# Kernel tuning notes

Measured on AMD Instinct MI355X. Metric: run time of the kernel, lower is better.

The kernel has to match this reference:

```python
import jax, jax.numpy as jnp
import numpy as np

DIM = 256          # args.dim
MAX_Z = 100        # args.max_z
N_ATOM_EMBED = DIM - 1  # Euclidean manifold: dim - 1
B, N = 256, 128    # graphs, nodes per graph
E = B * N * N      # fully connected edges per batch, flattened
NORM_CONSTANT = 1.0


def setup_inputs() -> dict:
    key = jax.random.key(0)
    ks = jax.random.split(key, 8)
    x = jax.random.normal(ks[0], (B, N, 3), dtype=jnp.float32)
    categories = jax.random.randint(ks[1], (B, N), 0, MAX_Z)
    charges = jax.random.normal(ks[2], (B, N, 1), dtype=jnp.float32)
    edges = jax.random.randint(ks[3], (2, E), 0, B * N)
    node_mask = jnp.ones((B, N, 1), dtype=jnp.float32)
    edge_mask = jnp.ones((E, 1), dtype=jnp.float32)
    # nn.Embedding(max_z, n_atom_embed, padding_idx=0): row 0 is zeros
    emb = jax.random.normal(ks[4], (MAX_Z, N_ATOM_EMBED), dtype=jnp.float32)
    emb_table = emb.at[0].set(0.0)
    # nn.Linear(dim, 2*dim)
    lim = 1.0 / np.sqrt(DIM)
    W = jax.random.uniform(ks[5], (DIM, 2 * DIM), minval=-lim, maxval=lim, dtype=jnp.float32)
    b_lin = jax.random.uniform(ks[6], (2 * DIM,), minval=-lim, maxval=lim, dtype=jnp.float32)
    return {"x": x, "categories": categories, "charges": charges, "edges": edges,
            "node_mask": node_mask, "edge_mask": edge_mask,
            "emb_table": emb_table, "W": W, "b_lin": b_lin}


def coord2diff(x, edges, norm_constant=NORM_CONSTANT):
    row, col = edges[0], edges[1]
    coord_diff = x[row] - x[col]                              # [E, 3] gather + diff
    radial = jnp.sum(coord_diff * coord_diff, axis=1, keepdims=True)  # [E, 1]
    norm = jnp.sqrt(radial + 1e-8)
    coord_diff = coord_diff / (norm + norm_constant)
    return radial, coord_diff


def reference(x, categories, charges, edges, node_mask, edge_mask, emb_table, W, b_lin):
    h = emb_table[categories]                      # [B, N, dim-1] embedding lookup
    h = jnp.concatenate([charges, h], axis=2)      # [B, N, dim]
    b, n_nodes, d = h.shape
    xf = x.reshape(b * n_nodes, 3)
    nm = node_mask.reshape(b * n_nodes, 1)
    h = h.reshape(b * n_nodes, d) * nm             # masked node features
    radial, coord_diff = coord2diff(xf, edges)     # edge-index gather + norm
    # encode() pass-through (abstract layers treated as identity), then head
    parameters = h @ W + b_lin                     # [B*N, 2*dim] mean/logvar
    return parameters, radial, coord_diff
```

## Files before the change

### kernel.cpp

```cpp
#include <hip/hip_runtime.h>

typedef unsigned short u16;
typedef unsigned int u32;
typedef __attribute__((ext_vector_type(8))) short bf16x8;
typedef __attribute__((ext_vector_type(4))) float f32x4;

#define DIM 256
#define NOUT 512
#define MROWS 32768
#define NNODE 32768
#define NEDGE (256*128*128)
#define PARAM_SZ (32768*512)
#define GEMM_BLOCKS 512
#define EDGE_BLOCKS 4096

__device__ __forceinline__ u16 f2bf(float f) {
    u32 x = __float_as_uint(f);
    u32 r = (x + 0x7FFFu + ((x >> 16) & 1u)) >> 16;
    return (u16)r;
}
__device__ __forceinline__ float bf2f(u16 u) {
    union { u32 i; float f; } v; v.i = ((u32)u) << 16; return v.f;
}

__global__ __launch_bounds__(256) void prep_kernel(const float* __restrict__ W,
                                                   const float* __restrict__ x,
                                                   const float* __restrict__ emb,
                                                   u16* __restrict__ Wt,
                                                   float4* __restrict__ xp,
                                                   u16* __restrict__ embp) {
    const int b = blockIdx.x;
    const int tid = threadIdx.x;
    if (b < 128) {
        __shared__ u16 tile[32][33];
        int k0 = (b >> 4) * 32;
        int n0 = (b & 15) * 32;
        int tx = tid & 31, ty0 = tid >> 5;
        #pragma unroll
        for (int j = 0; j < 4; ++j) {
            int ty = ty0 + j * 8;
            tile[ty][tx] = f2bf(W[(k0 + ty) * NOUT + n0 + tx]);
        }
        __syncthreads();
        #pragma unroll
        for (int j = 0; j < 4; ++j) {
            int ty = ty0 + j * 8;
            Wt[(n0 + ty) * DIM + k0 + tx] = tile[tx][ty];
        }
    } else if (b < 256) {
        int i = (b - 128) * 256 + tid;
        float4 v;
        v.x = x[i * 3 + 0]; v.y = x[i * 3 + 1]; v.z = x[i * 3 + 2]; v.w = 0.0f;
        xp[i] = v;
    } else {
        int i = (b - 256) * 256 + tid;
        int col = i & 255;
        int row = i >> 8;
        embp[i] = (col == 0) ? (u16)0 : f2bf(emb[row * 255 + col - 1]);
    }
}

__device__ __forceinline__ void gather8_sc0(const float4* p0, const float4* p1,
                                            const float4* p2, const float4* p3,
                                            const float4* p4, const float4* p5,
                                            const float4* p6, const float4* p7,
                                            f32x4& a0, f32x4& a1, f32x4& a2, f32x4& a3,
                                            f32x4& b0, f32x4& b1, f32x4& b2, f32x4& b3) {
    asm volatile(
        "global_load_dwordx4 %0, %8, off sc0\n\t"
        "global_load_dwordx4 %1, %9, off sc0\n\t"
        "global_load_dwordx4 %2, %10, off sc0\n\t"
        "global_load_dwordx4 %3, %11, off sc0\n\t"
        "global_load_dwordx4 %4, %12, off sc0\n\t"
        "global_load_dwordx4 %5, %13, off sc0\n\t"
        "global_load_dwordx4 %6, %14, off sc0\n\t"
        "global_load_dwordx4 %7, %15, off sc0\n\t"
        "s_waitcnt vmcnt(0)"
        : "=&v"(a0), "=&v"(a1), "=&v"(a2), "=&v"(a3),
          "=&v"(b0), "=&v"(b1), "=&v"(b2), "=&v"(b3)
        : "v"(p0), "v"(p1), "v"(p2), "v"(p3), "v"(p4), "v"(p5), "v"(p6), "v"(p7)
        : "memory");
}

__device__ __forceinline__ void edge_part(int eb, int tid,
                                          const int* __restrict__ edges,
                                          const float4* __restrict__ xp,
                                          float* __restrict__ radial_out,
                                          float* __restrict__ cd_out,
                                          float* buf ) {
    const int t4 = eb * 256 + tid;
    int4 r4 = ((const int4*)edges)[t4];
    int4 c4 = ((const int4*)(edges + NEDGE))[t4];

    f32x4 xr0, xr1, xr2, xr3, xc0, xc1, xc2, xc3;
    gather8_sc0(xp + r4.x, xp + r4.y, xp + r4.z, xp + r4.w,
                xp + c4.x, xp + c4.y, xp + c4.z, xp + c4.w,
                xr0, xr1, xr2, xr3, xc0, xc1, xc2, xc3);

    f32x4 rad;
    float cdv[12];
    #pragma unroll
    for (int e = 0; e < 4; ++e) {
        f32x4 a = (e == 0) ? xr0 : (e == 1) ? xr1 : (e == 2) ? xr2 : xr3;
        f32x4 b = (e == 0) ? xc0 : (e == 1) ? xc1 : (e == 2) ? xc2 : xc3;
        float dx = a.x - b.x, dy = a.y - b.y, dz = a.z - b.z;
        float r = dx * dx + dy * dy + dz * dz;
        float inv = 1.0f / (sqrtf(r + 1e-8f) + 1.0f);
        rad[e] = r;
        cdv[e * 3 + 0] = dx * inv;
        cdv[e * 3 + 1] = dy * inv;
        cdv[e * 3 + 2] = dz * inv;
    }
    __builtin_nontemporal_store(rad, ((f32x4*)radial_out) + t4);

    #pragma unroll
    for (int k = 0; k < 3; ++k)
        ((f32x4*)buf)[tid * 3 + k] = ((const f32x4*)cdv)[k];
    __syncthreads();
    f32x4* cdg = (f32x4*)(cd_out + (size_t)eb * 3072);
    #pragma unroll
    for (int k = 0; k < 3; ++k)
        __builtin_nontemporal_store(((const f32x4*)buf)[k * 256 + tid], cdg + k * 256 + tid);
}

__device__ __forceinline__ void gemm_part(int gb, int tid,
                                          const int* __restrict__ cats,
                                          const float* __restrict__ charges,
                                          const float* __restrict__ nmask,
                                          const u16* __restrict__ embp,
                                          const u16* __restrict__ Wt,
                                          const float* __restrict__ bias,
                                          float* __restrict__ out,
                                          u16 (*h_lds)[DIM + 8]) {
    const int m0 = gb * 64;

    {
        int r = tid >> 2;
        int q = tid & 3;
        int m = m0 + r;
        float mask = nmask[m];
        const uint4* src = (const uint4*)(embp + (size_t)cats[m] * 256 + q * 64);
        uint4 v[8];
        #pragma unroll
        for (int t = 0; t < 8; ++t) v[t] = src[t];
        if (mask != 1.0f) {
            #pragma unroll
            for (int t = 0; t < 8; ++t) {
                u32* w = (u32*)&v[t];
                #pragma unroll
                for (int j = 0; j < 4; ++j) {
                    u16 lo = f2bf(bf2f((u16)(w[j] & 0xFFFF)) * mask);
                    u16 hi = f2bf(bf2f((u16)(w[j] >> 16)) * mask);
                    w[j] = (u32)lo | ((u32)hi << 16);
                }
            }
        }
        if (q == 0) {
            u32* w0 = (u32*)&v[0];
            w0[0] = (w0[0] & 0xFFFF0000u) | (u32)f2bf(charges[m] * mask);
        }
        #pragma unroll
        for (int t = 0; t < 8; ++t)
            *(uint4*)&h_lds[r][q * 64 + t * 8] = v[t];
    }
    __syncthreads();

    const int wave = tid >> 6;
    const int lane = tid & 63;
    const int lrow = lane & 15;
    const int quad = lane >> 4;
    const int nbase = wave * 128;

    f32x4 acc[4][8];
    #pragma unroll
    for (int ms = 0; ms < 4; ++ms)
        #pragma unroll
        for (int nt = 0; nt < 8; ++nt) acc[ms][nt] = (f32x4)(0.0f);

    #pragma unroll
    for (int k0 = 0; k0 < DIM; k0 += 32) {
        bf16x8 a[4];
        #pragma unroll
        for (int ms = 0; ms < 4; ++ms)
            a[ms] = *(const bf16x8*)&h_lds[ms * 16 + lrow][k0 + quad * 8];
        #pragma unroll
        for (int nt = 0; nt < 8; ++nt) {
            bf16x8 bfr = *(const bf16x8*)&Wt[(size_t)(nbase + nt * 16 + lrow) * DIM + k0 + quad * 8];
            #pragma unroll
            for (int ms = 0; ms < 4; ++ms)
                acc[ms][nt] = __builtin_amdgcn_mfma_f32_16x16x32_bf16(a[ms], bfr, acc[ms][nt], 0, 0, 0);
        }
    }

    #pragma unroll
    for (int nt = 0; nt < 8; ++nt) {
        int n = nbase + nt * 16 + lrow;
        float bv = bias[n];
        #pragma unroll
        for (int ms = 0; ms < 4; ++ms)
            #pragma unroll
            for (int r = 0; r < 4; ++r)
                __builtin_nontemporal_store(acc[ms][nt][r] + bv,
                    out + (size_t)(m0 + ms * 16 + quad * 4 + r) * NOUT + n);
    }
}

__global__ __launch_bounds__(256, 2) void main_kernel(const int* __restrict__ cats,
                                                      const float* __restrict__ charges,
                                                      const float* __restrict__ nmask,
                                                      const u16* __restrict__ embp,
                                                      const u16* __restrict__ Wt,
                                                      const float* __restrict__ bias,
                                                      const int* __restrict__ edges,
                                                      const float4* __restrict__ xp,
                                                      float* __restrict__ params,
                                                      float* __restrict__ radial,
                                                      float* __restrict__ cd) {
    __shared__ char smem[64 * (DIM + 8) * sizeof(u16)];
    if (blockIdx.x < GEMM_BLOCKS)
        gemm_part(blockIdx.x, threadIdx.x, cats, charges, nmask, embp, Wt, bias, params,
                  (u16 (*)[DIM + 8])smem);
    else
        edge_part(blockIdx.x - GEMM_BLOCKS, threadIdx.x, edges, xp, radial, cd,
                  (float*)smem);
}

extern "C" void kernel_launch(void* const* d_in, const int* in_sizes, int n_in,
                              void* d_out, int out_size, void* d_ws, size_t ws_size,
                              hipStream_t stream) {
    const float* x       = (const float*)d_in[0];
    const int*   cats    = (const int*)d_in[1];
    const float* charges = (const float*)d_in[2];
    const int*   edges   = (const int*)d_in[3];
    const float* nmask   = (const float*)d_in[4];
    const float* emb     = (const float*)d_in[6];
    const float* W       = (const float*)d_in[7];
    const float* bias    = (const float*)d_in[8];

    float* out    = (float*)d_out;
    float* params = out;
    float* radial = out + PARAM_SZ;
    float* cd     = out + PARAM_SZ + NEDGE;

    u16*    Wt   = (u16*)d_ws;
    float4* xp   = (float4*)((char*)d_ws + 256 * 1024);
    u16*    embp = (u16*)((char*)d_ws + 768 * 1024);

    prep_kernel<<<356, 256, 0, stream>>>(W, x, emb, Wt, xp, embp);
    main_kernel<<<GEMM_BLOCKS + EDGE_BLOCKS, 256, 0, stream>>>(
        cats, charges, nmask, embp, Wt, bias, edges, xp, params, radial, cd);
}
```

Measured before the change: 232.7 us.

## Split fused GEMM/edge kernel into separate edge and GEMM launches

Replaces the single heterogeneous kernel, which branched on block index between GEMM and edge work, with two separate kernels launched back to back on the same stream. Each kernel now gets its own register allocation, LDS size and launch bounds, so the lightweight edge kernel is no longer limited by the GEMM's resource footprint and can reach higher occupancy. The cost is an extra launch and losing the overlap between GEMM and edge work within one grid.

```diff
diff --git a/kernel.cpp b/kernel.cpp
--- a/kernel.cpp
+++ b/kernel.cpp
@@ -82,12 +82,13 @@
         : "memory");
 }
 
-__device__ __forceinline__ void edge_part(int eb, int tid,
-                                          const int* __restrict__ edges,
-                                          const float4* __restrict__ xp,
-                                          float* __restrict__ radial_out,
-                                          float* __restrict__ cd_out,
-                                          float* buf ) {
+__global__ __launch_bounds__(256) void edge_kernel(const int* __restrict__ edges,
+                                                   const float4* __restrict__ xp,
+                                                   float* __restrict__ radial_out,
+                                                   float* __restrict__ cd_out) {
+    __shared__ float buf[3072];
+    const int eb = blockIdx.x;
+    const int tid = threadIdx.x;
     const int t4 = eb * 256 + tid;
     int4 r4 = ((const int4*)edges)[t4];
     int4 c4 = ((const int4*)(edges + NEDGE))[t4];
@@ -123,15 +124,16 @@
         __builtin_nontemporal_store(((const f32x4*)buf)[k * 256 + tid], cdg + k * 256 + tid);
 }
 
-__device__ __forceinline__ void gemm_part(int gb, int tid,
-                                          const int* __restrict__ cats,
-                                          const float* __restrict__ charges,
-                                          const float* __restrict__ nmask,
-                                          const u16* __restrict__ embp,
-                                          const u16* __restrict__ Wt,
-                                          const float* __restrict__ bias,
-                                          float* __restrict__ out,
-                                          u16 (*h_lds)[DIM + 8]) {
+__global__ __launch_bounds__(256, 2) void gemm_kernel(const int* __restrict__ cats,
+                                                      const float* __restrict__ charges,
+                                                      const float* __restrict__ nmask,
+                                                      const u16* __restrict__ embp,
+                                                      const u16* __restrict__ Wt,
+                                                      const float* __restrict__ bias,
+                                                      float* __restrict__ out) {
+    __shared__ u16 h_lds[64][DIM + 8];
+    const int gb = blockIdx.x;
+    const int tid = threadIdx.x;
     const int m0 = gb * 64;
 
     {
@@ -205,26 +207,6 @@
     }
 }
 
-__global__ __launch_bounds__(256, 2) void main_kernel(const int* __restrict__ cats,
-                                                      const float* __restrict__ charges,
-                                                      const float* __restrict__ nmask,
-                                                      const u16* __restrict__ embp,
-                                                      const u16* __restrict__ Wt,
-                                                      const float* __restrict__ bias,
-                                                      const int* __restrict__ edges,
-                                                      const float4* __restrict__ xp,
-                                                      float* __restrict__ params,
-                                                      float* __restrict__ radial,
-                                                      float* __restrict__ cd) {
-    __shared__ char smem[64 * (DIM + 8) * sizeof(u16)];
-    if (blockIdx.x < GEMM_BLOCKS)
-        gemm_part(blockIdx.x, threadIdx.x, cats, charges, nmask, embp, Wt, bias, params,
-                  (u16 (*)[DIM + 8])smem);
-    else
-        edge_part(blockIdx.x - GEMM_BLOCKS, threadIdx.x, edges, xp, radial, cd,
-                  (float*)smem);
-}
-
 extern "C" void kernel_launch(void* const* d_in, const int* in_sizes, int n_in,
                               void* d_out, int out_size, void* d_ws, size_t ws_size,
                               hipStream_t stream) {
@@ -247,6 +229,6 @@
     u16*    embp = (u16*)((char*)d_ws + 768 * 1024);
 
     prep_kernel<<<356, 256, 0, stream>>>(W, x, emb, Wt, xp, embp);
-    main_kernel<<<GEMM_BLOCKS + EDGE_BLOCKS, 256, 0, stream>>>(
-        cats, charges, nmask, embp, Wt, bias, edges, xp, params, radial, cd);
-}
+    edge_kernel<<<EDGE_BLOCKS, 256, 0, stream>>>(edges, xp, radial, cd);
+    gemm_kernel<<<GEMM_BLOCKS, 256, 0, stream>>>(cats, charges, nmask, embp, Wt, bias, params);
+}
```

Measured after the change: 235.6 us. Within noise of the previous version (+1.2%).
